# Kernel optimization log

Measured on AMD Instinct MI355X. Metric: run time of the kernel, lower is better.

Reference implementation:

```python
import jax, jax.numpy as jnp
import numpy as np

K = 3  # per_pix_kernel


def conv2d(x, w, b, pad):
    y = jax.lax.conv_general_dilated(
        x, w, window_strides=(1, 1), padding=[(pad, pad), (pad, pad)],
        dimension_numbers=('NCHW', 'OIHW', 'NCHW'))
    return y + b[None, :, None, None]


def per_pix_apply(x, kmap):
    # x: [B,C,H,W]; kmap: [B,K*K,H,W] (tanh-activated per-pixel kernels)
    # out[b,c,h,w] = sum_j patch_j(x)[b,c,h,w] * kmap[b,j,h,w]
    B, C, H, W = x.shape
    p = K // 2
    xp = jnp.pad(x, ((0, 0), (0, 0), (p, p), (p, p)))
    patches = jnp.stack(
        [xp[:, :, di:di + H, dj:dj + W] for di in range(K) for dj in range(K)],
        axis=1)  # [B, K*K, C, H, W]
    return jnp.einsum('bjchw,bjhw->bchw', patches, kmap)


def setup_inputs() -> dict:
    key = jax.random.key(0)
    ks = jax.random.split(key, 7)
    B, C, H, W = 4, 64, 256, 256
    kk = K * K  # 9
    s = 0.05
    return {
        'feature': jax.random.normal(ks[0], (B, C, H, W), jnp.float32),
        'w_sharp': jax.random.normal(ks[1], (kk, C, 5, 5), jnp.float32) * s,
        'b_sharp': jnp.zeros((kk,), jnp.float32),
        'w_r1': jax.random.normal(ks[2], (kk, C, 3, 3), jnp.float32) * s,
        'b_r1': jnp.zeros((kk,), jnp.float32),
        'w_r2': jax.random.normal(ks[3], (kk, kk, 3, 3), jnp.float32) * s,
        'b_r2': jnp.zeros((kk,), jnp.float32),
    }


def reference(feature, w_sharp, b_sharp, w_r1, b_r1, w_r2, b_r2):
    # sharp_attention = local_conv: 5x5 conv -> tanh -> per-pixel dynamic filter
    att_kernels = jnp.tanh(conv2d(feature, w_sharp, b_sharp, pad=2))  # [B,9,H,W]
    attention_feature = per_pix_apply(feature, att_kernels)           # [B,C,H,W]
    # reblur_filer (ratio == 1): conv3x3 -> conv3x3 -> tanh
    d = feature - attention_feature
    r = conv2d(d, w_r1, b_r1, pad=1)
    r = conv2d(r, w_r2, b_r2, pad=1)
    reblur_filter = jnp.tanh(r)  # [B,9,H,W]
    return reblur_filter, attention_feature
```

## Files before the change

### kernel.cpp

```cpp
#include <hip/hip_runtime.h>

#define B_ 4
#define C_ 64
#define H_ 256
#define W_ 256
#define KK 9

typedef __attribute__((ext_vector_type(8))) short short8;
typedef __attribute__((ext_vector_type(4))) float float4_;

static __device__ __forceinline__ unsigned short f2bf(float f) {
    unsigned int u = __builtin_bit_cast(unsigned int, f);
    unsigned int r = (u + 0x7fffu + ((u >> 16) & 1u)) >> 16;
    return (unsigned short)r;
}
static __device__ __forceinline__ float bf2f(short s) {
    return __builtin_bit_cast(float, (unsigned int)((unsigned short)s) << 16);
}
static __device__ __forceinline__ void gld16(const unsigned short* gp, unsigned short* lbase) {
    __builtin_amdgcn_global_load_lds(
        (const __attribute__((address_space(1))) unsigned int*)gp,
        (__attribute__((address_space(3))) unsigned int*)lbase, 16, 0, 0);
}

__global__ __launch_bounds__(256) void nchw2nhwc(
    const float* __restrict__ x, unsigned short* __restrict__ xh)
{
    __shared__ unsigned short t[256 * 66];
    int row = blockIdx.x;
    int b = row >> 8;
    const float* src = x + ((size_t)b * 64) * 65536 + (size_t)(row & 255) * 256;
    int tid = threadIdx.x;

    #pragma unroll 4
    for (int c = 0; c < 64; ++c)
        t[tid * 66 + c] = f2bf(src[(size_t)c * 65536 + tid]);
    __syncthreads();

    unsigned short* dst = xh + (size_t)row * 256 * 64;
    #pragma unroll
    for (int it = 0; it < 8; ++it) {
        int idx = it * 256 + tid;
        int pix = idx >> 3, g = idx & 7;
        short8 v = *(const short8*)(&t[pix * 66 + g * 8]);
        *(short8*)(dst + (size_t)pix * 64 + g * 8) = v;
    }
}

__global__ __launch_bounds__(256) void wprep_all(
    const float* __restrict__ w5, const float* __restrict__ w3,
    unsigned short* __restrict__ wb, unsigned short* __restrict__ wb3)
{
    int i = blockIdx.x * 256 + threadIdx.x;
    if (i < 25600) {
        int tap = i >> 10;
        int q = (i >> 7) & 7;
        int n = (i >> 3) & 15;
        int e = i & 7;
        int c = q * 8 + e;
        int di = tap / 5, dj = tap % 5;
        float v = (n < KK) ? w5[((n * C_ + c) * 5 + di) * 5 + dj] : 0.f;
        wb[i] = f2bf(v);
    } else if (i < 34816) {
        int k = i - 25600;
        int tap = k >> 10;
        int q = (k >> 7) & 7;
        int n = (k >> 3) & 15;
        int e = k & 7;
        int c = q * 8 + e;
        int di = tap / 3, dj = tap % 3;
        float v = (n < KK) ? w3[((n * C_ + c) * 3 + di) * 3 + dj] : 0.f;
        wb3[k] = f2bf(v);
    }
}

static __device__ __forceinline__ void stage20(
    const unsigned short* __restrict__ xh, unsigned short* xs,
    int b, int h0, int w0, bool interior, int tid)
{
    if (interior) {
        int lane = tid & 63, wid = tid >> 6;
        int p = (lane & 7) ^ ((lane >> 3) & 7);
        int sub = lane >> 3;
        for (int it = wid; it < 50; it += 4) {
            int pix = it * 8 + sub;
            int py = pix / 20, px = pix % 20;
            int gy = h0 + py - 2, gx = w0 + px - 2;
            const unsigned short* g = xh + ((size_t)((b * 256 + gy) * 256 + gx) * 64 + p * 8);
            gld16(g, &xs[it * 512]);
        }
    } else {
        for (int q = tid; q < 400 * 8; q += 256) {
            int p = q & 7;
            int pix = q >> 3;
            int py = pix / 20, px = pix % 20;
            int gy = h0 + py - 2, gx = w0 + px - 2;
            short8 v = (short8)0;
            if (gy >= 0 && gy < H_ && gx >= 0 && gx < W_)
                v = *(const short8*)(xh + ((size_t)((b * 256 + gy) * 256 + gx) * 64 + p * 8));
            *(short8*)(&xs[(pix << 6) + ((p ^ (pix & 7)) << 3)]) = v;
        }
    }
}

__global__ __launch_bounds__(256) void conv5_mfma(
    const unsigned short* __restrict__ xh,
    const unsigned short* __restrict__ wb,
    const float* __restrict__ bias,
    unsigned short* __restrict__ att)
{
    __shared__ unsigned short xs[20 * 20 * 64];

    int tid = threadIdx.x;
    int bx = blockIdx.x & 15;
    int by = (blockIdx.x >> 4) & 15;
    int b  = blockIdx.x >> 8;
    int h0 = by * 16, w0 = bx * 16;
    bool interior = (bx >= 1 && bx <= 14 && by >= 1 && by <= 14);

    stage20(xh, xs, b, h0, w0, interior, tid);
    __syncthreads();

    int lane = tid & 63;
    int wid  = tid >> 6;
    int m16  = lane & 15;
    int lq   = lane >> 4;

    float4_ acc[4];
    float bj = (m16 < KK) ? bias[m16] : 0.f;
    #pragma unroll
    for (int r = 0; r < 4; ++r) acc[r] = (float4_){bj, bj, bj, bj};

    #pragma unroll
    for (int dj = 0; dj < 5; ++dj) {
        short8 bfr[5][2];
        #pragma unroll
        for (int di = 0; di < 5; ++di) {
            int tap = di * 5 + dj;
            bfr[di][0] = *(const short8*)(wb + (((tap * 8 + lq) * 16 + m16) * 8));
            bfr[di][1] = *(const short8*)(wb + (((tap * 8 + 4 + lq) * 16 + m16) * 8));
        }
        int px = m16 + dj;
        #pragma unroll
        for (int s = 0; s < 8; ++s) {
            int pix = (wid * 4 + s) * 20 + px;
            int c0 = lq ^ (pix & 7);
            short8 a0 = *(const short8*)(&xs[(pix << 6) + (c0 << 3)]);
            short8 a1 = *(const short8*)(&xs[(pix << 6) + ((c0 ^ 4) << 3)]);
            #pragma unroll
            for (int di = 0; di < 5; ++di) {
                int r = s - di;
                if (r < 0 || r > 3) continue;
                acc[r] = __builtin_amdgcn_mfma_f32_16x16x32_bf16(a0, bfr[di][0], acc[r], 0, 0, 0);
                acc[r] = __builtin_amdgcn_mfma_f32_16x16x32_bf16(a1, bfr[di][1], acc[r], 0, 0, 0);
            }
        }
    }

    if (m16 < KK) {
        #pragma unroll
        for (int r = 0; r < 4; ++r) {
            int py = h0 + wid * 4 + r;
            #pragma unroll
            for (int reg = 0; reg < 4; ++reg) {
                int px = w0 + lq * 4 + reg;
                att[((b * KK + m16) << 16) | (py << 8) | px] = f2bf(tanhf(acc[r][reg]));
            }
        }
    }
}

__global__ __launch_bounds__(256) void conv3_fused(
    const unsigned short* __restrict__ xh,
    const unsigned short* __restrict__ att,
    const unsigned short* __restrict__ wb3,
    const float* __restrict__ bias,
    float* __restrict__ attf,
    unsigned short* __restrict__ r1h)
{
    __shared__ unsigned short xs[20 * 20 * 64];

    int tid = threadIdx.x;
    int bx = blockIdx.x & 15;
    int by = (blockIdx.x >> 4) & 15;
    int b  = blockIdx.x >> 8;
    int h0 = by * 16, w0 = bx * 16;
    bool interior = (bx >= 1 && bx <= 14 && by >= 1 && by <= 14);

    stage20(xh, xs, b, h0, w0, interior, tid);
    __syncthreads();

    short8 dreg[11];
    #pragma unroll
    for (int it = 0; it < 11; ++it) {
        dreg[it] = (short8)0;
        int idx = it * 256 + tid;
        if (idx < 2592) {
            int g = idx & 7;
            int pix = idx >> 3;
            int py = pix / 18, px = pix % 18;
            int gy = h0 + py - 1, gx = w0 + px - 1;
            if (gy >= 0 && gy < H_ && gx >= 0 && gx < W_) {
                int hw = (gy << 8) | gx;
                float a[KK];
                #pragma unroll
                for (int j = 0; j < KK; ++j)
                    a[j] = bf2f(att[((b * KK + j) << 16) | hw]);

                float s[8] = {0, 0, 0, 0, 0, 0, 0, 0};
                float xc[8];
                #pragma unroll
                for (int di = 0; di < 3; ++di) {
                    #pragma unroll
                    for (int dj = 0; dj < 3; ++dj) {
                        int pix20 = (py + di) * 20 + (px + dj);
                        int c = g ^ (pix20 & 7);
                        short8 v = *(const short8*)(&xs[(pix20 << 6) + (c << 3)]);
                        float aj = a[di * 3 + dj];
                        #pragma unroll
                        for (int i = 0; i < 8; ++i) {
                            float xv = bf2f(v[i]);
                            s[i] += xv * aj;
                            if (di == 1 && dj == 1) xc[i] = xv;
                        }
                    }
                }
                if (py >= 1 && py <= 16 && px >= 1 && px <= 16) {
                    #pragma unroll
                    for (int i = 0; i < 8; ++i)
                        attf[((b * C_ + g * 8 + i) << 16) | hw] = s[i];
                }
                short8 dv;
                #pragma unroll
                for (int i = 0; i < 8; ++i) dv[i] = (short)f2bf(xc[i] - s[i]);
                dreg[it] = dv;
            }
        }
    }
    __syncthreads();

    #pragma unroll
    for (int it = 0; it < 11; ++it) {
        int idx = it * 256 + tid;
        if (idx < 2592) {
            int g = idx & 7;
            int pix = idx >> 3;
            *(short8*)(&xs[(pix << 6) + ((g ^ (pix & 7)) << 3)]) = dreg[it];
        }
    }
    __syncthreads();

    int lane = tid & 63;
    int wid  = tid >> 6;
    int m16  = lane & 15;
    int lq   = lane >> 4;

    float4_ acc[4];
    float bj = (m16 < KK) ? bias[m16] : 0.f;
    #pragma unroll
    for (int r = 0; r < 4; ++r) acc[r] = (float4_){bj, bj, bj, bj};

    #pragma unroll
    for (int dj = 0; dj < 3; ++dj) {
        short8 bfr[3][2];
        #pragma unroll
        for (int di = 0; di < 3; ++di) {
            int tap = di * 3 + dj;
            bfr[di][0] = *(const short8*)(wb3 + (((tap * 8 + lq) * 16 + m16) * 8));
            bfr[di][1] = *(const short8*)(wb3 + (((tap * 8 + 4 + lq) * 16 + m16) * 8));
        }
        int px = m16 + dj;
        #pragma unroll
        for (int s = 0; s < 6; ++s) {
            int pix = (wid * 4 + s) * 18 + px;
            int c0 = lq ^ (pix & 7);
            short8 a0 = *(const short8*)(&xs[(pix << 6) + (c0 << 3)]);
            short8 a1 = *(const short8*)(&xs[(pix << 6) + ((c0 ^ 4) << 3)]);
            #pragma unroll
            for (int di = 0; di < 3; ++di) {
                int r = s - di;
                if (r < 0 || r > 3) continue;
                acc[r] = __builtin_amdgcn_mfma_f32_16x16x32_bf16(a0, bfr[di][0], acc[r], 0, 0, 0);
                acc[r] = __builtin_amdgcn_mfma_f32_16x16x32_bf16(a1, bfr[di][1], acc[r], 0, 0, 0);
            }
        }
    }

    if (m16 < KK) {
        #pragma unroll
        for (int r = 0; r < 4; ++r) {
            int py = h0 + wid * 4 + r;
            #pragma unroll
            for (int reg = 0; reg < 4; ++reg) {
                int px = w0 + lq * 4 + reg;
                r1h[((b * KK + m16) << 16) | (py << 8) | px] = f2bf(acc[r][reg]);
            }
        }
    }
}

__global__ __launch_bounds__(256) void conv3_tanh9(
    const unsigned short* __restrict__ r1h, const float* __restrict__ w,
    const float* __restrict__ bias, float* __restrict__ out)
{
    const int TW = 32, TH = 8, PW = 34, PH = 10;
    __shared__ float lds[KK][PH][PW];

    int tid = threadIdx.x;
    int tx = tid & 31, ty = tid >> 5;
    int bw = blockIdx.x & 7;
    int bh = (blockIdx.x >> 3) & 31;
    int b  = blockIdx.x >> 8;
    int h0 = bh * TH, w0 = bw * TW;

    for (int idx = tid; idx < KK * PH * PW; idx += 256) {
        int px = idx % PW;
        int py = (idx / PW) % PH;
        int ch = idx / (PW * PH);
        int gy = h0 + py - 1, gx = w0 + px - 1;
        float v = 0.f;
        if (gy >= 0 && gy < H_ && gx >= 0 && gx < W_)
            v = bf2f(r1h[((b * KK + ch) << 16) | (gy << 8) | gx]);
        lds[ch][py][px] = v;
    }
    __syncthreads();

    float acc[KK];
    #pragma unroll
    for (int j = 0; j < KK; ++j) acc[j] = bias[j];

    for (int cin = 0; cin < KK; ++cin) {
        #pragma unroll
        for (int di = 0; di < 3; ++di) {
            #pragma unroll
            for (int dj = 0; dj < 3; ++dj) {
                float xv = lds[cin][ty + di][tx + dj];
                #pragma unroll
                for (int j = 0; j < KK; ++j)
                    acc[j] += xv * w[((j * KK + cin) * 3 + di) * 3 + dj];
            }
        }
    }

    int h = h0 + ty, wq = w0 + tx;
    #pragma unroll
    for (int j = 0; j < KK; ++j)
        out[((b * KK + j) << 16) | (h << 8) | wq] = tanhf(acc[j]);
}

extern "C" void kernel_launch(void* const* d_in, const int* in_sizes, int n_in,
                              void* d_out, int out_size, void* d_ws, size_t ws_size,
                              hipStream_t stream) {
    const float* feature = (const float*)d_in[0];
    const float* w_sharp = (const float*)d_in[1];
    const float* b_sharp = (const float*)d_in[2];
    const float* w_r1    = (const float*)d_in[3];
    const float* b_r1    = (const float*)d_in[4];
    const float* w_r2    = (const float*)d_in[5];
    const float* b_r2    = (const float*)d_in[6];

    float* out_reblur = (float*)d_out;
    float* out_attf   = out_reblur + (size_t)B_ * KK * H_ * W_;

    char* ws = (char*)d_ws;
    unsigned short* xh   = (unsigned short*)ws;
    unsigned short* wb   = (unsigned short*)(ws + 33554432);
    unsigned short* wb3  = (unsigned short*)(ws + 33619968);
    unsigned short* att  = (unsigned short*)(ws + 33652736);
    unsigned short* r1h  = (unsigned short*)(ws + 38371328);

    nchw2nhwc<<<1024, 256, 0, stream>>>(feature, xh);
    wprep_all<<<136, 256, 0, stream>>>(w_sharp, w_r1, wb, wb3);
    conv5_mfma<<<1024, 256, 0, stream>>>(xh, wb, b_sharp, att);
    conv3_fused<<<1024, 256, 0, stream>>>(xh, att, wb3, b_r1, out_attf, r1h);
    conv3_tanh9<<<1024, 256, 0, stream>>>(r1h, w_r2, b_r2, out_reblur);
}
```

Before: 118.0 us.

## Read dynamic-filter taps from global/L2 and stage attention maps in LDS

In the fused conv3 kernel, the 20x20x64 LDS staging of the input feature is replaced by direct global loads of the 3x3 neighbourhood for each pixel/channel-group, relying on cache reuse. The 9 attention-kernel planes for the 18x18 halo are staged into a small LDS buffer, so each thread reads them with one vector load instead of nine strided global loads. The difference tile is written straight into a separate LDS buffer, which removes the register array and one barrier. LDS use and register pressure go down, which could raise occupancy, but each thread now issues up to nine global loads with boundary branches instead of LDS reads.

```diff
diff --git a/kernel.cpp b/kernel.cpp
--- a/kernel.cpp
+++ b/kernel.cpp
@@ -109,7 +109,7 @@
     const float* __restrict__ bias,
     unsigned short* __restrict__ att)
 {
-    __shared__ unsigned short xs[20 * 20 * 64];
+    __shared__ __align__(16) unsigned short xs[20 * 20 * 64];
 
     int tid = threadIdx.x;
     int bx = blockIdx.x & 15;
@@ -178,75 +178,70 @@
     float* __restrict__ attf,
     unsigned short* __restrict__ r1h)
 {
-    __shared__ unsigned short xs[20 * 20 * 64];
+    __shared__ __align__(16) unsigned short ds[324 * 64];
+    __shared__ __align__(16) unsigned short att_s[324 * 16];
 
     int tid = threadIdx.x;
     int bx = blockIdx.x & 15;
     int by = (blockIdx.x >> 4) & 15;
     int b  = blockIdx.x >> 8;
     int h0 = by * 16, w0 = bx * 16;
-    bool interior = (bx >= 1 && bx <= 14 && by >= 1 && by <= 14);
-
-    stage20(xh, xs, b, h0, w0, interior, tid);
-    __syncthreads();
-
-    short8 dreg[11];
+
+    for (int idx = tid; idx < 2916; idx += 256) {
+        int j = idx / 324;
+        int pix = idx - j * 324;
+        int py = pix / 18, px = pix - py * 18;
+        int gy = h0 + py - 1, gx = w0 + px - 1;
+        unsigned short v = 0;
+        if (gy >= 0 && gy < H_ && gx >= 0 && gx < W_)
+            v = att[((b * KK + j) << 16) | (gy << 8) | gx];
+        att_s[pix * 16 + j] = v;
+    }
+    __syncthreads();
+
     #pragma unroll
     for (int it = 0; it < 11; ++it) {
-        dreg[it] = (short8)0;
         int idx = it * 256 + tid;
-        if (idx < 2592) {
-            int g = idx & 7;
-            int pix = idx >> 3;
-            int py = pix / 18, px = pix % 18;
-            int gy = h0 + py - 1, gx = w0 + px - 1;
-            if (gy >= 0 && gy < H_ && gx >= 0 && gx < W_) {
-                int hw = (gy << 8) | gx;
-                float a[KK];
+        if (idx >= 2592) break;
+        int g = idx & 7;
+        int pix = idx >> 3;
+        int py = pix / 18, px = pix - py * 18;
+        int gy = h0 + py - 1, gx = w0 + px - 1;
+        short8 dv = (short8)0;
+        if (gy >= 0 && gy < H_ && gx >= 0 && gx < W_) {
+            int hw = (gy << 8) | gx;
+            short8 av = *(const short8*)(&att_s[pix * 16]);
+            float a8 = bf2f(att_s[pix * 16 + 8]);
+
+            float s[8] = {0, 0, 0, 0, 0, 0, 0, 0};
+            float xc[8] = {0, 0, 0, 0, 0, 0, 0, 0};
+            #pragma unroll
+            for (int di = 0; di < 3; ++di) {
+                int y = gy + di - 1;
                 #pragma unroll
-                for (int j = 0; j < KK; ++j)
-                    a[j] = bf2f(att[((b * KK + j) << 16) | hw]);
-
-                float s[8] = {0, 0, 0, 0, 0, 0, 0, 0};
-                float xc[8];
-                #pragma unroll
-                for (int di = 0; di < 3; ++di) {
+                for (int dj = 0; dj < 3; ++dj) {
+                    int xq = gx + dj - 1;
+                    if (y < 0 || y >= H_ || xq < 0 || xq >= W_) continue;
+                    short8 v = *(const short8*)(xh + ((size_t)((b << 16) | (y << 8) | xq) * 64 + g * 8));
+                    int t9 = di * 3 + dj;
+                    float aj = (t9 < 8) ? bf2f(av[t9]) : a8;
                     #pragma unroll
-                    for (int dj = 0; dj < 3; ++dj) {
-                        int pix20 = (py + di) * 20 + (px + dj);
-                        int c = g ^ (pix20 & 7);
-                        short8 v = *(const short8*)(&xs[(pix20 << 6) + (c << 3)]);
-                        float aj = a[di * 3 + dj];
-                        #pragma unroll
-                        for (int i = 0; i < 8; ++i) {
-                            float xv = bf2f(v[i]);
-                            s[i] += xv * aj;
-                            if (di == 1 && dj == 1) xc[i] = xv;
-                        }
+                    for (int i = 0; i < 8; ++i) {
+                        float xv = bf2f(v[i]);
+                        s[i] += xv * aj;
+                        if (di == 1 && dj == 1) xc[i] = xv;
                     }
                 }
-                if (py >= 1 && py <= 16 && px >= 1 && px <= 16) {
-                    #pragma unroll
-                    for (int i = 0; i < 8; ++i)
-                        attf[((b * C_ + g * 8 + i) << 16) | hw] = s[i];
-                }
-                short8 dv;
+            }
+            if (py >= 1 && py <= 16 && px >= 1 && px <= 16) {
                 #pragma unroll
-                for (int i = 0; i < 8; ++i) dv[i] = (short)f2bf(xc[i] - s[i]);
-                dreg[it] = dv;
-            }
-        }
-    }
-    __syncthreads();
-
-    #pragma unroll
-    for (int it = 0; it < 11; ++it) {
-        int idx = it * 256 + tid;
-        if (idx < 2592) {
-            int g = idx & 7;
-            int pix = idx >> 3;
-            *(short8*)(&xs[(pix << 6) + ((g ^ (pix & 7)) << 3)]) = dreg[it];
-        }
+                for (int i = 0; i < 8; ++i)
+                    attf[((b * C_ + g * 8 + i) << 16) | hw] = s[i];
+            }
+            #pragma unroll
+            for (int i = 0; i < 8; ++i) dv[i] = (short)f2bf(xc[i] - s[i]);
+        }
+        *(short8*)(&ds[(pix << 6) + ((g ^ (pix & 7)) << 3)]) = dv;
     }
     __syncthreads();
 
@@ -274,8 +269,8 @@
         for (int s = 0; s < 6; ++s) {
             int pix = (wid * 4 + s) * 18 + px;
             int c0 = lq ^ (pix & 7);
-            short8 a0 = *(const short8*)(&xs[(pix << 6) + (c0 << 3)]);
-            short8 a1 = *(const short8*)(&xs[(pix << 6) + ((c0 ^ 4) << 3)]);
+            short8 a0 = *(const short8*)(&ds[(pix << 6) + (c0 << 3)]);
+            short8 a1 = *(const short8*)(&ds[(pix << 6) + ((c0 ^ 4) << 3)]);
             #pragma unroll
             for (int di = 0; di < 3; ++di) {
                 int r = s - di;
```

New measurement: 158.3 us. +34.2%, slower.

## Stage 18x18 halo and attention kernels in LDS for fused conv3 kernel

Applied to the files above, without the earlier changes.

The fused attention/conv3 kernel now stages only an 18x18 feature halo instead of 20x20, using async global-to-LDS loads for interior tiles. It also preloads the nine per-pixel attention weights for the tile into shared memory rather than reading them per thread from global memory. Ring pixels whose 3x3 neighbourhood falls outside the staged tile read their missing neighbours directly from global memory. This cuts LDS footprint and staging traffic and removes redundant attention loads, at the cost of a divergent slow path for border pixels.

```diff
diff --git a/kernel.cpp b/kernel.cpp
--- a/kernel.cpp
+++ b/kernel.cpp
@@ -109,7 +109,7 @@
     const float* __restrict__ bias,
     unsigned short* __restrict__ att)
 {
-    __shared__ unsigned short xs[20 * 20 * 64];
+    __shared__ __align__(16) unsigned short xs[20 * 20 * 64];
 
     int tid = threadIdx.x;
     int bx = blockIdx.x & 15;
@@ -178,7 +178,8 @@
     float* __restrict__ attf,
     unsigned short* __restrict__ r1h)
 {
-    __shared__ unsigned short xs[20 * 20 * 64];
+    __shared__ __align__(16) unsigned short xs[328 * 64];
+    __shared__ unsigned short att_s[324 * 9];
 
     int tid = threadIdx.x;
     int bx = blockIdx.x & 15;
@@ -187,7 +188,39 @@
     int h0 = by * 16, w0 = bx * 16;
     bool interior = (bx >= 1 && bx <= 14 && by >= 1 && by <= 14);
 
-    stage20(xh, xs, b, h0, w0, interior, tid);
+    for (int idx = tid; idx < 2916; idx += 256) {
+        int j = idx / 324;
+        int pix = idx - j * 324;
+        int py = pix / 18, px = pix - py * 18;
+        int gy = h0 + py - 1, gx = w0 + px - 1;
+        unsigned short v = 0;
+        if (gy >= 0 && gy < H_ && gx >= 0 && gx < W_)
+            v = att[((b * KK + j) << 16) | (gy << 8) | gx];
+        att_s[pix * 9 + j] = v;
+    }
+    if (interior) {
+        int lane = tid & 63, wid = tid >> 6;
+        int p = (lane & 7) ^ ((lane >> 3) & 7);
+        int sub = lane >> 3;
+        for (int it = wid; it < 41; it += 4) {
+            int pix = it * 8 + sub;
+            int py = pix / 18, px = pix - py * 18;
+            int gy = h0 + py - 1, gx = w0 + px - 1;
+            const unsigned short* g = xh + ((size_t)((b * 256 + gy) * 256 + gx) * 64 + p * 8);
+            gld16(g, &xs[it * 512]);
+        }
+    } else {
+        for (int q = tid; q < 324 * 8; q += 256) {
+            int p = q & 7;
+            int pix = q >> 3;
+            int py = pix / 18, px = pix - py * 18;
+            int gy = h0 + py - 1, gx = w0 + px - 1;
+            short8 v = (short8)0;
+            if (gy >= 0 && gy < H_ && gx >= 0 && gx < W_)
+                v = *(const short8*)(xh + ((size_t)((b * 256 + gy) * 256 + gx) * 64 + p * 8));
+            *(short8*)(&xs[(pix << 6) + ((p ^ (pix & 7)) << 3)]) = v;
+        }
+    }
     __syncthreads();
 
     short8 dreg[11];
@@ -198,37 +231,61 @@
         if (idx < 2592) {
             int g = idx & 7;
             int pix = idx >> 3;
-            int py = pix / 18, px = pix % 18;
+            int py = pix / 18, px = pix - py * 18;
             int gy = h0 + py - 1, gx = w0 + px - 1;
             if (gy >= 0 && gy < H_ && gx >= 0 && gx < W_) {
-                int hw = (gy << 8) | gx;
                 float a[KK];
                 #pragma unroll
-                for (int j = 0; j < KK; ++j)
-                    a[j] = bf2f(att[((b * KK + j) << 16) | hw]);
+                for (int j = 0; j < KK; ++j) a[j] = bf2f(att_s[pix * 9 + j]);
 
                 float s[8] = {0, 0, 0, 0, 0, 0, 0, 0};
-                float xc[8];
-                #pragma unroll
-                for (int di = 0; di < 3; ++di) {
+                float xc[8] = {0, 0, 0, 0, 0, 0, 0, 0};
+                if (py >= 1 && py <= 16 && px >= 1 && px <= 16) {
                     #pragma unroll
-                    for (int dj = 0; dj < 3; ++dj) {
-                        int pix20 = (py + di) * 20 + (px + dj);
-                        int c = g ^ (pix20 & 7);
-                        short8 v = *(const short8*)(&xs[(pix20 << 6) + (c << 3)]);
-                        float aj = a[di * 3 + dj];
+                    for (int di = 0; di < 3; ++di) {
                         #pragma unroll
-                        for (int i = 0; i < 8; ++i) {
-                            float xv = bf2f(v[i]);
-                            s[i] += xv * aj;
-                            if (di == 1 && dj == 1) xc[i] = xv;
+                        for (int dj = 0; dj < 3; ++dj) {
+                            int tp = (py + di - 1) * 18 + (px + dj - 1);
+                            int c = g ^ (tp & 7);
+                            short8 v = *(const short8*)(&xs[(tp << 6) + (c << 3)]);
+                            float aj = a[di * 3 + dj];
+                            #pragma unroll
+                            for (int i = 0; i < 8; ++i) {
+                                float xv = bf2f(v[i]);
+                                s[i] += xv * aj;
+                                if (di == 1 && dj == 1) xc[i] = xv;
+                            }
                         }
                     }
-                }
-                if (py >= 1 && py <= 16 && px >= 1 && px <= 16) {
+                    int hw = (gy << 8) | gx;
                     #pragma unroll
                     for (int i = 0; i < 8; ++i)
                         attf[((b * C_ + g * 8 + i) << 16) | hw] = s[i];
+                } else {
+                    #pragma unroll
+                    for (int di = 0; di < 3; ++di) {
+                        #pragma unroll
+                        for (int dj = 0; dj < 3; ++dj) {
+                            int tpy = py + di - 1, tpx = px + dj - 1;
+                            short8 v = (short8)0;
+                            if (tpy >= 0 && tpy < 18 && tpx >= 0 && tpx < 18) {
+                                int tp = tpy * 18 + tpx;
+                                int c = g ^ (tp & 7);
+                                v = *(const short8*)(&xs[(tp << 6) + (c << 3)]);
+                            } else {
+                                int gyt = h0 + tpy - 1, gxt = w0 + tpx - 1;
+                                if (gyt >= 0 && gyt < H_ && gxt >= 0 && gxt < W_)
+                                    v = *(const short8*)(xh + ((size_t)((b * 256 + gyt) * 256 + gxt) * 64 + g * 8));
+                            }
+                            float aj = a[di * 3 + dj];
+                            #pragma unroll
+                            for (int i = 0; i < 8; ++i) {
+                                float xv = bf2f(v[i]);
+                                s[i] += xv * aj;
+                                if (di == 1 && dj == 1) xc[i] = xv;
+                            }
+                        }
+                    }
                 }
                 short8 dv;
                 #pragma unroll
```

Result: slower. 136.9 us (+16.0%).
